# Optimization experiments

Hardware: AMD Instinct MI355X
Metric: run time of the kernel (lower is better)

Reference implementation:

```python
import jax, jax.numpy as jnp
import numpy as np

MASK_NUM = -2.0 ** 32 + 1.0  # additive mask value from the module


def setup_inputs() -> dict:
    key = jax.random.key(0)
    k1, k2, k3, k4 = jax.random.split(key, 4)
    BH, S, D = 32, 2048, 64   # batch*heads, seq, head_dim
    B = 2                      # true batch for key padding masks
    q = jax.random.normal(k1, (BH, S, D), dtype=jnp.float32)
    k = jax.random.normal(k2, (BH, S, D), dtype=jnp.float32)
    v = jax.random.normal(k3, (BH, S, D), dtype=jnp.float32)
    masks = jax.random.randint(k4, (B, S), 0, 2, dtype=jnp.int32)  # 1 = masked key
    return {"q": q, "k": k, "v": v, "masks": masks}


def reference(q, k, v, masks):
    # scores: [BH, Sq, Sk]
    d = q.shape[-1]
    scores = jnp.einsum("bqd,bkd->bqk", q, k) / jnp.sqrt(jnp.float32(d))
    # tile key-padding masks over heads: [B,Sk] -> [BH,Sk], add big negative
    tile = q.shape[0] // masks.shape[0]
    m = jnp.tile(masks.astype(jnp.float32), (tile, 1))  # [BH, Sk]
    scores = scores + m[:, None, :] * MASK_NUM
    attn = jax.nn.softmax(scores, axis=-1)
    # dropout rate is 0.0 -> identity
    out = jnp.einsum("bqk,bkd->bqd", attn, v)
    return out
```

## Files before the change

kernel.cpp:

```cpp
#include <hip/hip_runtime.h>
#include <hip/hip_bf16.h>


#define SQ 2048
#define DD 64
#define NT 32

typedef __attribute__((ext_vector_type(8)))  short bf16x8;
typedef __attribute__((ext_vector_type(16))) float f32x16;
typedef __attribute__((ext_vector_type(2)))  unsigned uint2v;

#define LOG2E  1.4426950408889634f
#define QSCALE (0.125f * LOG2E)
#define MASKV  (-4294967295.0f * LOG2E)
#define THRL   (8.0f * LOG2E)

__device__ __forceinline__ int cvt_pk(float lo, float hi) {
    int r;
    asm("v_cvt_pk_bf16_f32 %0, %1, %2" : "=v"(r) : "v"(lo), "v"(hi));
    return r;
}
__device__ __forceinline__ int koff(int c, int e) {
    return c * 1024 + ((e ^ (((c & 3) << 1) | (e >> 5))) << 4);
}
__device__ __forceinline__ float xmax(float x) {
#if __has_builtin(__builtin_amdgcn_permlane32_swap)
    union { float f; unsigned u; } a; a.f = x;
    uint2v r = __builtin_amdgcn_permlane32_swap(a.u, a.u, false, false);
    union { unsigned u; float f; } p0, p1; p0.u = r[0]; p1.u = r[1];
    return fmaxf(p0.f, p1.f);
#else
    return fmaxf(x, __shfl_xor(x, 32));
#endif
}
__device__ __forceinline__ float xsum(float x) {
#if __has_builtin(__builtin_amdgcn_permlane32_swap)
    union { float f; unsigned u; } a; a.f = x;
    uint2v r = __builtin_amdgcn_permlane32_swap(a.u, a.u, false, false);
    union { unsigned u; float f; } p0, p1; p0.u = r[0]; p1.u = r[1];
    return p0.f + p1.f;
#else
    return x + __shfl_xor(x, 32);
#endif
}
__device__ __forceinline__ void plswap2(unsigned a, unsigned b,
                                        unsigned& lo01, unsigned& hi23, int hi) {
#if __has_builtin(__builtin_amdgcn_permlane32_swap)
    uint2v r = __builtin_amdgcn_permlane32_swap(a, b, false, false);
    lo01 = r[0]; hi23 = r[1];
#else
    unsigned pa = (unsigned)__shfl_xor((int)a, 32);
    unsigned pb = (unsigned)__shfl_xor((int)b, 32);
    lo01 = hi ? pb : a;
    hi23 = hi ? b : pa;
#endif
}

__global__ __launch_bounds__(256, 2) void attn_fwd(
    const float* __restrict__ q, const float* __restrict__ k,
    const float* __restrict__ v, const int* __restrict__ masks,
    float* __restrict__ out)
{
    __shared__ alignas(16) char smem[40960];
    float* Mf = (float*)(smem + 32768);

    const int x    = blockIdx.x;
    const int orig = (x & 7) * 64 + (x >> 3);
    const int h    = orig >> 4;
    const int qb   = orig & 15;
    const int tid  = threadIdx.x;
    const int w    = tid >> 6;
    const int lane = tid & 63;
    const int l31  = lane & 31;
    const int hi   = lane >> 5;

    const float* __restrict__ qh = q + (size_t)h * SQ * DD;
    const float* __restrict__ kh = k + (size_t)h * SQ * DD;
    const float* __restrict__ vh = v + (size_t)h * SQ * DD;
    const int*   __restrict__ mrow = masks + (h & 1) * SQ;

    {
        int4 a = *(const int4*)(mrow + tid * 8);
        int4 b = *(const int4*)(mrow + tid * 8 + 4);
        float4 fa = { a.x ? MASKV : 0.f, a.y ? MASKV : 0.f,
                      a.z ? MASKV : 0.f, a.w ? MASKV : 0.f };
        float4 fb = { b.x ? MASKV : 0.f, b.y ? MASKV : 0.f,
                      b.z ? MASKV : 0.f, b.w ? MASKV : 0.f };
        *(float4*)(Mf + tid * 8)     = fa;
        *(float4*)(Mf + tid * 8 + 4) = fb;
    }

    const int qrow = qb * 128 + w * 32 + l31;
    bf16x8 qf[4];
#pragma unroll
    for (int dc = 0; dc < 4; ++dc) {
        const float* p = qh + (size_t)qrow * DD + dc * 16 + hi * 8;
        float4 a = *(const float4*)p;
        float4 b = *(const float4*)(p + 4);
        union { int i[4]; bf16x8 v; } f;
        f.i[0] = cvt_pk(a.x * QSCALE, a.y * QSCALE);
        f.i[1] = cvt_pk(a.z * QSCALE, a.w * QSCALE);
        f.i[2] = cvt_pk(b.x * QSCALE, b.y * QSCALE);
        f.i[3] = cvt_pk(b.z * QSCALE, b.w * QSCALE);
        qf[dc] = f.v;
    }

    f32x16 o[2];
#pragma unroll
    for (int dt = 0; dt < 2; ++dt)
#pragma unroll
      for (int i = 0; i < 16; ++i) o[dt][i] = 0.f;
    float m = -3.0e38f, l = 0.f;

    const int rK = tid >> 3, cK = tid & 7;
    const int aV = tid & 31, dV = (tid >> 5) * 8;
    const int eK = ((cK & 1) << 5) | rK;
    const int kA_off = koff(cK >> 1,       eK);
    const int kB_off = koff(4 + (cK >> 1), eK);

    float4 kA0, kA1, kB0, kB1, vA0, vA1, vB0, vB1;
#define LOADKV(kt)                                                        \
    {   const float* kpA = kh + (size_t)((kt) + rK) * DD + 8 * cK;       \
        const float* kpB = kpA + 32 * DD;                                 \
        const float* vpA = vh + (size_t)((kt) + 2 * aV) * DD + dV;       \
        const float* vpB = vpA + DD;                                      \
        kA0 = *(const float4*)kpA; kA1 = *(const float4*)(kpA + 4);      \
        kB0 = *(const float4*)kpB; kB1 = *(const float4*)(kpB + 4);      \
        vA0 = *(const float4*)vpA; vA1 = *(const float4*)(vpA + 4);      \
        vB0 = *(const float4*)vpB; vB1 = *(const float4*)(vpB + 4);      }

#define WRITEKV(Kp, Vp)                                                   \
    {   union { int i[4]; bf16x8 b; } kw;                                 \
        kw.i[0] = cvt_pk(kA0.x, kA0.y); kw.i[1] = cvt_pk(kA0.z, kA0.w);  \
        kw.i[2] = cvt_pk(kA1.x, kA1.y); kw.i[3] = cvt_pk(kA1.z, kA1.w);  \
        *(bf16x8*)((Kp) + kA_off) = kw.b;                                 \
        kw.i[0] = cvt_pk(kB0.x, kB0.y); kw.i[1] = cvt_pk(kB0.z, kB0.w);  \
        kw.i[2] = cvt_pk(kB1.x, kB1.y); kw.i[3] = cvt_pk(kB1.z, kB1.w);  \
        *(bf16x8*)((Kp) + kB_off) = kw.b;                                 \
        float va[8] = {vA0.x, vA0.y, vA0.z, vA0.w, vA1.x, vA1.y, vA1.z, vA1.w}; \
        float vb[8] = {vB0.x, vB0.y, vB0.z, vB0.w, vB1.x, vB1.y, vB1.z, vB1.w}; \
        _Pragma("unroll")                                                 \
        for (int j = 0; j < 8; ++j) {                                     \
            const int r_ = dV + j;                                        \
            const int cv_ = ((aV >> 3) << 1) | (r_ >> 5);                 \
            const int ev_ = (((aV >> 2) & 1) << 5) | (r_ & 31);           \
            *(unsigned*)((Vp) + koff(cv_, ev_) + 4 * (aV & 3))            \
                = (unsigned)cvt_pk(va[j], vb[j]);                         \
        }                                                                 }

    LOADKV(0)
    WRITEKV(smem, smem + 8192)
    __syncthreads();

    int boff = 0;
    for (int it = 0; it < NT; ++it) {
        const int kt = it * 64;
        const bool more = (it + 1 < NT);
        if (more) LOADKV(kt + 64)
        char* Kb = smem + boff;
        char* Vb = Kb + 8192;

        const float* mf = Mf + kt;
        f32x16 s0, s1;
#pragma unroll
        for (int g = 0; g < 4; ++g) {
            float4 m0 = *(const float4*)(mf + 8 * g + 4 * hi);
            float4 m1 = *(const float4*)(mf + 32 + 8 * g + 4 * hi);
            s0[4*g+0] = m0.x; s0[4*g+1] = m0.y; s0[4*g+2] = m0.z; s0[4*g+3] = m0.w;
            s1[4*g+0] = m1.x; s1[4*g+1] = m1.y; s1[4*g+2] = m1.z; s1[4*g+3] = m1.w;
        }
        __builtin_amdgcn_s_setprio(1);
#pragma unroll
        for (int dc = 0; dc < 4; ++dc) {
            bf16x8 k0 = *(const bf16x8*)(Kb + koff(dc,     lane));
            bf16x8 k1 = *(const bf16x8*)(Kb + koff(4 + dc, lane));
            s0 = __builtin_amdgcn_mfma_f32_32x32x16_bf16(k0, qf[dc], s0, 0, 0, 0);
            s1 = __builtin_amdgcn_mfma_f32_32x32x16_bf16(k1, qf[dc], s1, 0, 0, 0);
        }
        __builtin_amdgcn_s_setprio(0);

        float t[16];
#pragma unroll
        for (int i = 0; i < 16; ++i) t[i] = fmaxf(s0[i], s1[i]);
#pragma unroll
        for (int stp = 8; stp >= 1; stp >>= 1)
#pragma unroll
            for (int i = 0; i < stp; ++i) t[i] = fmaxf(t[i], t[i + stp]);
        float pmax = xmax(t[0]);

        float mn = m;
        if (!__all(pmax <= m + THRL)) {
            mn = fmaxf(m, pmax);
            float al = __builtin_amdgcn_exp2f(m - mn);
            l *= al;
#pragma unroll
            for (int dt = 0; dt < 2; ++dt)
#pragma unroll
              for (int i = 0; i < 16; ++i) o[dt][i] *= al;
            m = mn;
        }

        float p0[16], p1[16];
#pragma unroll
        for (int i = 0; i < 16; ++i) {
            p0[i] = __builtin_amdgcn_exp2f(s0[i] - mn);
            p1[i] = __builtin_amdgcn_exp2f(s1[i] - mn);
        }
        float u[16];
#pragma unroll
        for (int i = 0; i < 16; ++i) u[i] = p0[i] + p1[i];
#pragma unroll
        for (int stp = 8; stp >= 1; stp >>= 1)
#pragma unroll
            for (int i = 0; i < stp; ++i) u[i] += u[i + stp];
        l += xsum(u[0]);

        unsigned pk[2][4][2];
#pragma unroll
        for (int g = 0; g < 4; ++g) {
            pk[0][g][0] = (unsigned)cvt_pk(p0[4*g+0], p0[4*g+1]);
            pk[0][g][1] = (unsigned)cvt_pk(p0[4*g+2], p0[4*g+3]);
            pk[1][g][0] = (unsigned)cvt_pk(p1[4*g+0], p1[4*g+1]);
            pk[1][g][1] = (unsigned)cvt_pk(p1[4*g+2], p1[4*g+3]);
        }

        if (more) {
            char* Kn = smem + (boff ^ 16384);
            WRITEKV(Kn, Kn + 8192)
        }

        __builtin_amdgcn_s_setprio(1);
#pragma unroll
        for (int kc = 0; kc < 4; ++kc) {
            const int kb = kc >> 1, kp = kc & 1;
            union { unsigned u[4]; bf16x8 b; } pu;
            unsigned lo0, hi0, lo1, hi1;
            plswap2(pk[kb][2*kp][0], pk[kb][2*kp+1][0], lo0, hi0, hi);
            plswap2(pk[kb][2*kp][1], pk[kb][2*kp+1][1], lo1, hi1, hi);
            pu.u[0] = lo0; pu.u[1] = lo1; pu.u[2] = hi0; pu.u[3] = hi1;
#pragma unroll
            for (int dt = 0; dt < 2; ++dt) {
                bf16x8 vf = *(const bf16x8*)(Vb + koff(kc * 2 + dt, lane));
                o[dt] = __builtin_amdgcn_mfma_f32_32x32x16_bf16(vf, pu.b, o[dt], 0, 0, 0);
            }
        }
        __builtin_amdgcn_s_setprio(0);

        __syncthreads();
        boff ^= 16384;
    }

    const float invl = 1.0f / l;
    float* op = out + (size_t)h * SQ * DD + (size_t)qrow * DD;
#pragma unroll
    for (int dt = 0; dt < 2; ++dt)
#pragma unroll
      for (int g = 0; g < 4; ++g) {
        float4 r = { o[dt][4*g+0] * invl, o[dt][4*g+1] * invl,
                     o[dt][4*g+2] * invl, o[dt][4*g+3] * invl };
        *(float4*)(op + 32 * dt + 8 * g + 4 * hi) = r;
      }
}

extern "C" void kernel_launch(void* const* d_in, const int* in_sizes, int n_in,
                              void* d_out, int out_size, void* d_ws, size_t ws_size,
                              hipStream_t stream) {
    const float* q = (const float*)d_in[0];
    const float* k = (const float*)d_in[1];
    const float* v = (const float*)d_in[2];
    const int* masks = (const int*)d_in[3];
    float* out = (float*)d_out;
    attn_fwd<<<dim3(512), dim3(256), 0, stream>>>(q, k, v, masks, out);
}
```

Measured before the change: 62.56 us.

## Split key range across two wave groups per block and merge softmax partials

Doubles the block to 512 threads so two groups of four waves each process half of the key sequence for the same 128 query rows, then combine partial max, sum and output through shared memory at the end. The mask is now read directly from global memory per tile instead of being precomputed into shared memory. This is meant to raise parallelism and shorten each block's serial loop over 32 tiles, at the cost of 64KB shared memory, a final reduction step with an extra barrier, and higher register and occupancy pressure.

```diff
diff --git a/kernel.cpp b/kernel.cpp
--- a/kernel.cpp
+++ b/kernel.cpp
@@ -4,7 +4,7 @@
 
 #define SQ 2048
 #define DD 64
-#define NT 32
+#define NT2 16
 
 typedef __attribute__((ext_vector_type(8)))  short bf16x8;
 typedef __attribute__((ext_vector_type(16))) float f32x16;
@@ -56,39 +56,31 @@
 #endif
 }
 
-__global__ __launch_bounds__(256, 2) void attn_fwd(
+__global__ __launch_bounds__(512, 4) void attn_fwd(
     const float* __restrict__ q, const float* __restrict__ k,
     const float* __restrict__ v, const int* __restrict__ masks,
     float* __restrict__ out)
 {
-    __shared__ alignas(16) char smem[40960];
-    float* Mf = (float*)(smem + 32768);
+    __shared__ alignas(16) char smem[65536];
 
     const int x    = blockIdx.x;
     const int orig = (x & 7) * 64 + (x >> 3);
     const int h    = orig >> 4;
     const int qb   = orig & 15;
     const int tid  = threadIdx.x;
-    const int w    = tid >> 6;
+    const int w8   = tid >> 6;
+    const int half = w8 >> 2;
+    const int w    = w8 & 3;
     const int lane = tid & 63;
     const int l31  = lane & 31;
     const int hi   = lane >> 5;
+    const int lt   = tid & 255;
+    const int kb0  = half << 10;
 
     const float* __restrict__ qh = q + (size_t)h * SQ * DD;
     const float* __restrict__ kh = k + (size_t)h * SQ * DD;
     const float* __restrict__ vh = v + (size_t)h * SQ * DD;
     const int*   __restrict__ mrow = masks + (h & 1) * SQ;
-
-    {
-        int4 a = *(const int4*)(mrow + tid * 8);
-        int4 b = *(const int4*)(mrow + tid * 8 + 4);
-        float4 fa = { a.x ? MASKV : 0.f, a.y ? MASKV : 0.f,
-                      a.z ? MASKV : 0.f, a.w ? MASKV : 0.f };
-        float4 fb = { b.x ? MASKV : 0.f, b.y ? MASKV : 0.f,
-                      b.z ? MASKV : 0.f, b.w ? MASKV : 0.f };
-        *(float4*)(Mf + tid * 8)     = fa;
-        *(float4*)(Mf + tid * 8 + 4) = fb;
-    }
 
     const int qrow = qb * 128 + w * 32 + l31;
     bf16x8 qf[4];
@@ -112,11 +104,12 @@
       for (int i = 0; i < 16; ++i) o[dt][i] = 0.f;
     float m = -3.0e38f, l = 0.f;
 
-    const int rK = tid >> 3, cK = tid & 7;
-    const int aV = tid & 31, dV = (tid >> 5) * 8;
+    const int rK = lt >> 3, cK = lt & 7;
+    const int aV = lt & 31, dV = (lt >> 5) * 8;
     const int eK = ((cK & 1) << 5) | rK;
     const int kA_off = koff(cK >> 1,       eK);
     const int kB_off = koff(4 + (cK >> 1), eK);
+    char* const Hb = smem + (half << 15);
 
     float4 kA0, kA1, kB0, kB1, vA0, vA1, vB0, vB1;
 #define LOADKV(kt)                                                        \
@@ -148,26 +141,28 @@
                 = (unsigned)cvt_pk(va[j], vb[j]);                         \
         }                                                                 }
 
-    LOADKV(0)
-    WRITEKV(smem, smem + 8192)
+    LOADKV(kb0)
+    WRITEKV(Hb, Hb + 8192)
     __syncthreads();
 
     int boff = 0;
-    for (int it = 0; it < NT; ++it) {
-        const int kt = it * 64;
-        const bool more = (it + 1 < NT);
+    for (int it = 0; it < NT2; ++it) {
+        const int kt = kb0 + it * 64;
+        const bool more = (it + 1 < NT2);
         if (more) LOADKV(kt + 64)
-        char* Kb = smem + boff;
+        char* Kb = Hb + boff;
         char* Vb = Kb + 8192;
 
-        const float* mf = Mf + kt;
+        const int* mk = mrow + kt + 4 * hi;
         f32x16 s0, s1;
 #pragma unroll
         for (int g = 0; g < 4; ++g) {
-            float4 m0 = *(const float4*)(mf + 8 * g + 4 * hi);
-            float4 m1 = *(const float4*)(mf + 32 + 8 * g + 4 * hi);
-            s0[4*g+0] = m0.x; s0[4*g+1] = m0.y; s0[4*g+2] = m0.z; s0[4*g+3] = m0.w;
-            s1[4*g+0] = m1.x; s1[4*g+1] = m1.y; s1[4*g+2] = m1.z; s1[4*g+3] = m1.w;
+            int4 a = *(const int4*)(mk + 8 * g);
+            int4 b = *(const int4*)(mk + 32 + 8 * g);
+            s0[4*g+0] = a.x ? MASKV : 0.f; s0[4*g+1] = a.y ? MASKV : 0.f;
+            s0[4*g+2] = a.z ? MASKV : 0.f; s0[4*g+3] = a.w ? MASKV : 0.f;
+            s1[4*g+0] = b.x ? MASKV : 0.f; s1[4*g+1] = b.y ? MASKV : 0.f;
+            s1[4*g+2] = b.z ? MASKV : 0.f; s1[4*g+3] = b.w ? MASKV : 0.f;
         }
         __builtin_amdgcn_s_setprio(1);
 #pragma unroll
@@ -200,15 +195,14 @@
             m = mn;
         }
 
-        float p0[16], p1[16];
 #pragma unroll
         for (int i = 0; i < 16; ++i) {
-            p0[i] = __builtin_amdgcn_exp2f(s0[i] - mn);
-            p1[i] = __builtin_amdgcn_exp2f(s1[i] - mn);
+            s0[i] = __builtin_amdgcn_exp2f(s0[i] - mn);
+            s1[i] = __builtin_amdgcn_exp2f(s1[i] - mn);
         }
         float u[16];
 #pragma unroll
-        for (int i = 0; i < 16; ++i) u[i] = p0[i] + p1[i];
+        for (int i = 0; i < 16; ++i) u[i] = s0[i] + s1[i];
 #pragma unroll
         for (int stp = 8; stp >= 1; stp >>= 1)
 #pragma unroll
@@ -218,14 +212,14 @@
         unsigned pk[2][4][2];
 #pragma unroll
         for (int g = 0; g < 4; ++g) {
-            pk[0][g][0] = (unsigned)cvt_pk(p0[4*g+0], p0[4*g+1]);
-            pk[0][g][1] = (unsigned)cvt_pk(p0[4*g+2], p0[4*g+3]);
-            pk[1][g][0] = (unsigned)cvt_pk(p1[4*g+0], p1[4*g+1]);
-            pk[1][g][1] = (unsigned)cvt_pk(p1[4*g+2], p1[4*g+3]);
+            pk[0][g][0] = (unsigned)cvt_pk(s0[4*g+0], s0[4*g+1]);
+            pk[0][g][1] = (unsigned)cvt_pk(s0[4*g+2], s0[4*g+3]);
+            pk[1][g][0] = (unsigned)cvt_pk(s1[4*g+0], s1[4*g+1]);
+            pk[1][g][1] = (unsigned)cvt_pk(s1[4*g+2], s1[4*g+3]);
         }
 
         if (more) {
-            char* Kn = smem + (boff ^ 16384);
+            char* Kn = Hb + (boff ^ 16384);
             WRITEKV(Kn, Kn + 8192)
         }
 
@@ -250,16 +244,37 @@
         boff ^= 16384;
     }
 
-    const float invl = 1.0f / l;
-    float* op = out + (size_t)h * SQ * DD + (size_t)qrow * DD;
-#pragma unroll
-    for (int dt = 0; dt < 2; ++dt)
-#pragma unroll
-      for (int g = 0; g < 4; ++g) {
-        float4 r = { o[dt][4*g+0] * invl, o[dt][4*g+1] * invl,
-                     o[dt][4*g+2] * invl, o[dt][4*g+3] * invl };
-        *(float4*)(op + 32 * dt + 8 * g + 4 * hi) = r;
-      }
+    float* pr = (float*)(smem + w * 8704);
+    if (half) {
+#pragma unroll
+        for (int dt = 0; dt < 2; ++dt)
+#pragma unroll
+          for (int i = 0; i < 16; ++i)
+            pr[(dt * 16 + i) * 64 + lane] = o[dt][i];
+        pr[2048 + lane] = m;
+        pr[2112 + lane] = l;
+    }
+    __syncthreads();
+    if (!half) {
+        const float m1 = pr[2048 + lane];
+        const float l1 = pr[2112 + lane];
+        const float M  = fmaxf(m, m1);
+        const float a0 = __builtin_amdgcn_exp2f(m - M);
+        const float a1 = __builtin_amdgcn_exp2f(m1 - M);
+        const float invl = 1.0f / (a0 * l + a1 * l1);
+        float* op = out + (size_t)h * SQ * DD + (size_t)qrow * DD;
+#pragma unroll
+        for (int dt = 0; dt < 2; ++dt)
+#pragma unroll
+          for (int g = 0; g < 4; ++g) {
+            float4 r;
+            r.x = (a0 * o[dt][4*g+0] + a1 * pr[(dt*16 + 4*g+0) * 64 + lane]) * invl;
+            r.y = (a0 * o[dt][4*g+1] + a1 * pr[(dt*16 + 4*g+1) * 64 + lane]) * invl;
+            r.z = (a0 * o[dt][4*g+2] + a1 * pr[(dt*16 + 4*g+2) * 64 + lane]) * invl;
+            r.w = (a0 * o[dt][4*g+3] + a1 * pr[(dt*16 + 4*g+3) * 64 + lane]) * invl;
+            *(float4*)(op + 32 * dt + 8 * g + 4 * hi) = r;
+          }
+    }
 }
 
 extern "C" void kernel_launch(void* const* d_in, const int* in_sizes, int n_in,
@@ -270,5 +285,5 @@
     const float* v = (const float*)d_in[2];
     const int* masks = (const int*)d_in[3];
     float* out = (float*)d_out;
-    attn_fwd<<<dim3(512), dim3(256), 0, stream>>>(q, k, v, masks, out);
-}
+    attn_fwd<<<dim3(512), dim3(512), 0, stream>>>(q, k, v, masks, out);
+}
```

Result: slower. 135.2 us (+116.1%).
